# Kernel optimization log

Hardware: AMD Instinct MI355X
Metric: run time of the kernel (lower is better)

The kernel has to match this reference:

```python
import jax, jax.numpy as jnp
import numpy as np

N_NODES = 50000

def gcn_conv(x, src, dst, W, b):
    # x: [N, F_in], src/dst: [E], W: [F_in, F_out], b: [F_out]
    n = x.shape[0]
    xw = x @ W  # [N, F_out]
    # degree including self-loop (counted on destination nodes, PyG convention)
    deg = jax.ops.segment_sum(jnp.ones(src.shape[0], xw.dtype), dst, num_segments=n) + 1.0
    dinv = jax.lax.rsqrt(deg)  # deg >= 1 always
    norm = dinv[src] * dinv[dst]  # [E]
    msgs = xw[src] * norm[:, None]  # [E, F_out] gather + scale
    agg = jax.ops.segment_sum(msgs, dst, num_segments=n)  # scatter-add
    agg = agg + xw * (dinv * dinv)[:, None]  # self-loop contribution
    return agg + b


def setup_inputs() -> dict:
    key = jax.random.key(0)
    ks = jax.random.split(key, 8)
    n, e = N_NODES, 800000
    c_in, c_hid, c_out = 128, 128, 64
    x = jax.random.normal(ks[0], (n, c_in), dtype=jnp.float32)
    edge_index = jax.random.randint(ks[1], (2, e), 0, n, dtype=jnp.int64)
    s = 1.0 / np.sqrt(c_in)
    W1 = jax.random.uniform(ks[2], (c_in, c_hid), jnp.float32, -s, s)
    b1 = jnp.zeros((c_hid,), jnp.float32)
    sh = 1.0 / np.sqrt(c_hid)
    W2 = jax.random.uniform(ks[3], (c_hid, c_hid), jnp.float32, -sh, sh)
    b2 = jnp.zeros((c_hid,), jnp.float32)
    W3 = jax.random.uniform(ks[4], (c_hid, c_out), jnp.float32, -sh, sh)
    b3 = jnp.zeros((c_out,), jnp.float32)
    return {"x": x, "edge_index": edge_index, "W1": W1, "b1": b1,
            "W2": W2, "b2": b2, "W3": W3, "b3": b3}


def reference(x, edge_index, W1, b1, W2, b2, W3, b3):
    src, dst = edge_index[0], edge_index[1]
    h = gcn_conv(x, src, dst, W1, b1)
    h = gcn_conv(h, src, dst, W2, b2)
    h = gcn_conv(h, src, dst, W3, b3)
    return jax.nn.relu(h)  # activation applied after last layer only
```

## Files before the change

### kernel.cpp

```cpp
#include <hip/hip_runtime.h>
#include <hip/hip_fp16.h>


#define C_IN 128
#define C_HID 128
#define C_OUT 64
#define PART_BLOCKS 256
#define GEMM_BLOCKS 1024


__global__ __launch_bounds__(256) void buk_hist_kernel(const int* __restrict__ dst, int E,
                                                       int* __restrict__ bukCnt) {
    __shared__ int h[256];
    int tid = threadIdx.x;
    h[tid] = 0;
    __syncthreads();
    int chunk = (E + gridDim.x - 1) / gridDim.x;
    int lo = blockIdx.x * chunk;
    int hi = min(lo + chunk, E);
    for (int e = lo + tid; e < hi; e += 256)
        atomicAdd(&h[dst[e] >> 8], 1);
    __syncthreads();
    if (h[tid] > 0) atomicAdd(&bukCnt[tid], h[tid]);
}

__global__ __launch_bounds__(256) void buk_scan_kernel(const int* __restrict__ bukCnt,
                                                       int nbuk, int E,
                                                       int* __restrict__ bbase,
                                                       int* __restrict__ cursor) {
    __shared__ int lds[256];
    int tid = threadIdx.x;
    int v = (tid < nbuk) ? bukCnt[tid] : 0;
    lds[tid] = v;
    __syncthreads();
    for (int off = 1; off < 256; off <<= 1) {
        int u = (tid >= off) ? lds[tid - off] : 0;
        __syncthreads();
        lds[tid] += u;
        __syncthreads();
    }
    int ex = lds[tid] - v;
    if (tid < nbuk) { bbase[tid] = ex; cursor[tid] = ex; }
    if (tid == 0) bbase[nbuk] = E;
}

__global__ __launch_bounds__(256) void buk_place_kernel(const int* __restrict__ src,
                                                        const int* __restrict__ dst, int E,
                                                        int* __restrict__ cursor,
                                                        int2* __restrict__ ebuf) {
    __shared__ int h[256];
    __shared__ int base[256];
    __shared__ int c2[256];
    int tid = threadIdx.x;
    h[tid] = 0;
    c2[tid] = 0;
    __syncthreads();
    int chunk = (E + gridDim.x - 1) / gridDim.x;
    int lo = blockIdx.x * chunk;
    int hi = min(lo + chunk, E);
    for (int e = lo + tid; e < hi; e += 256)
        atomicAdd(&h[dst[e] >> 8], 1);
    __syncthreads();
    int cnt = h[tid];
    if (cnt > 0) base[tid] = atomicAdd(&cursor[tid], cnt);
    __syncthreads();
    for (int e = lo + tid; e < hi; e += 256) {
        int d = dst[e];
        int b = d >> 8;
        int slot = base[b] + atomicAdd(&c2[b], 1);
        ebuf[slot] = make_int2(src[e], d);
    }
}

__global__ __launch_bounds__(256) void buk_fill_kernel(const int2* __restrict__ ebuf,
                                                       const int* __restrict__ bbase,
                                                       int n, int E,
                                                       int* __restrict__ rowptr,
                                                       float* __restrict__ dinv,
                                                       int* __restrict__ csr) {
    __shared__ int deg[256];
    __shared__ int lds[256];
    int b = blockIdx.x;
    int tid = threadIdx.x;
    int lo = bbase[b];
    int hi = bbase[b + 1];
    int node0 = b << 8;
    deg[tid] = 0;
    __syncthreads();
    for (int e = lo + tid; e < hi; e += 256)
        atomicAdd(&deg[ebuf[e].y & 255], 1);
    __syncthreads();
    int d = deg[tid];
    lds[tid] = d;
    __syncthreads();
    for (int off = 1; off < 256; off <<= 1) {
        int u = (tid >= off) ? lds[tid - off] : 0;
        __syncthreads();
        lds[tid] += u;
        __syncthreads();
    }
    int ex = lds[tid] - d;
    int node = node0 + tid;
    if (node < n) {
        rowptr[node] = lo + ex;
        dinv[node] = rsqrtf((float)d + 1.0f);
    }
    if (tid == 0)
        rowptr[min(node0 + 256, n)] = hi;
    __syncthreads();
    deg[tid] = lo + ex;
    __syncthreads();
    for (int e = lo + tid; e < hi; e += 256) {
        int2 ed = ebuf[e];
        int slot = atomicAdd(&deg[ed.y & 255], 1);
        csr[slot] = ed.x;
    }
}

template <int FOUT>
__global__ __launch_bounds__(256, 4) void gemm_k128(const float* __restrict__ X,
                                                    const float* __restrict__ W,
                                                    const float* __restrict__ dinv,
                                                    float* __restrict__ Y,
                                                    __half* __restrict__ Yh, int n) {
    constexpr int K = 128;
    constexpr int CT = 64;
    constexpr int MT = 64;
    constexpr int NQ = CT / 4;
    constexpr int RPT = 4;
    constexpr int CTILES = FOUT / CT;
    __shared__ float Ws[K][CT];

    int tid = threadIdx.x;
    int ct = (CTILES == 1) ? 0 : (blockIdx.x & (CTILES - 1));
    int col0 = ct * CT;

#pragma unroll
    for (int i = 0; i < (K * CT / 4) / 256; ++i) {
        int idx = tid + i * 256;
        int k = idx / (CT / 4);
        int c = idx % (CT / 4);
        *(float4*)&Ws[k][c * 4] = *(const float4*)(W + (size_t)k * FOUT + col0 + c * 4);
    }
    __syncthreads();

    int cq = tid % NQ;
    int rg = tid / NQ;
    int nRowTiles = (n + MT - 1) / MT;
    int rtStride = gridDim.x / CTILES;

    for (int rt = blockIdx.x / CTILES; rt < nRowTiles; rt += rtStride) {
        int r0 = rt * MT + rg * RPT;

        const float* xb[RPT];
#pragma unroll
        for (int r = 0; r < RPT; ++r) {
            int gr = r0 + r;
            if (gr > n - 1) gr = n - 1;
            xb[r] = X + (size_t)gr * K;
        }

        float acc[RPT][4] = {};
        float4 xa[RPT];
#pragma unroll
        for (int r = 0; r < RPT; ++r) xa[r] = *(const float4*)(xb[r]);

#pragma unroll 2
        for (int k4 = 0; k4 < K / 4; ++k4) {
            float4 xn[RPT];
            if (k4 + 1 < K / 4) {
#pragma unroll
                for (int r = 0; r < RPT; ++r)
                    xn[r] = *(const float4*)(xb[r] + (k4 + 1) * 4);
            }
#pragma unroll
            for (int kk = 0; kk < 4; ++kk) {
                float4 w = *(float4*)&Ws[k4 * 4 + kk][cq * 4];
#pragma unroll
                for (int r = 0; r < RPT; ++r) {
                    float xarr[4] = {xa[r].x, xa[r].y, xa[r].z, xa[r].w};
                    float xv = xarr[kk];
                    acc[r][0] = fmaf(xv, w.x, acc[r][0]);
                    acc[r][1] = fmaf(xv, w.y, acc[r][1]);
                    acc[r][2] = fmaf(xv, w.z, acc[r][2]);
                    acc[r][3] = fmaf(xv, w.w, acc[r][3]);
                }
            }
#pragma unroll
            for (int r = 0; r < RPT; ++r) xa[r] = xn[r];
        }
#pragma unroll
        for (int r = 0; r < RPT; ++r) {
            int gr = r0 + r;
            if (gr < n) {
                size_t off = (size_t)gr * FOUT + col0 + cq * 4;
                *(float4*)(Y + off) =
                    make_float4(acc[r][0], acc[r][1], acc[r][2], acc[r][3]);
                float di = dinv[gr];
                __half2 h01 = __floats2half2_rn(acc[r][0] * di, acc[r][1] * di);
                __half2 h23 = __floats2half2_rn(acc[r][2] * di, acc[r][3] * di);
                uint2 pk = make_uint2(*(unsigned int*)&h01, *(unsigned int*)&h23);
                *(uint2*)(Yh + off) = pk;
            }
        }
    }
}

template <int NB, bool MASK>
__device__ __forceinline__ void batch_f128(const int* __restrict__ csr, int j, int rem,
                                           const __half* __restrict__ xwh, int lane,
                                           float2* acc) {
    int s[NB];
#pragma unroll
    for (int k = 0; k < NB; ++k) {
        int jj = MASK ? (j + ((k < rem) ? k : 0)) : (j + k);
        s[k] = csr[jj];
    }
    float2 v[NB];
#pragma unroll
    for (int k = 0; k < NB; ++k) {
        __half2 hv = ((const __half2*)(xwh + (size_t)s[k] * 128))[lane];
        v[k] = __half22float2(hv);
    }
#pragma unroll
    for (int k = 0; k < NB; ++k) {
        float m = (!MASK || (k < rem)) ? 1.0f : 0.0f;
        acc[k & 3].x = fmaf(v[k].x, m, acc[k & 3].x);
        acc[k & 3].y = fmaf(v[k].y, m, acc[k & 3].y);
    }
}

template <int NB, bool MASK>
__device__ __forceinline__ void batch_f64(const int* __restrict__ csr, int j, int rem,
                                          const __half* __restrict__ xwh, int lane,
                                          float* acc) {
    int s[NB];
#pragma unroll
    for (int k = 0; k < NB; ++k) {
        int jj = MASK ? (j + ((k < rem) ? k : 0)) : (j + k);
        s[k] = csr[jj];
    }
    float v[NB];
#pragma unroll
    for (int k = 0; k < NB; ++k)
        v[k] = __half2float(xwh[(size_t)s[k] * 64 + lane]);
#pragma unroll
    for (int k = 0; k < NB; ++k) {
        float m = (!MASK || (k < rem)) ? 1.0f : 0.0f;
        acc[k & 3] = fmaf(v[k], m, acc[k & 3]);
    }
}

template <int F, bool RELU>
__global__ __launch_bounds__(256) void agg_kernel(const int* __restrict__ rowptr,
                                                  const int* __restrict__ csr,
                                                  const float* __restrict__ xw,
                                                  const __half* __restrict__ xwh,
                                                  const float* __restrict__ dinv,
                                                  const float* __restrict__ bias,
                                                  float* __restrict__ out, int n) {
    int wave = threadIdx.x >> 6;
    int lane = threadIdx.x & 63;
    int i0 = blockIdx.x * 4 + wave;
    if (i0 >= n) return;
    int i = __builtin_amdgcn_readfirstlane(i0);
    float di = dinv[i];
    float d2 = di * di;
    int j = rowptr[i];
    int end = rowptr[i + 1];
    j = __builtin_amdgcn_readfirstlane(j);
    end = __builtin_amdgcn_readfirstlane(end);

    if constexpr (F == 128) {
        float2 x0 = ((const float2*)(xw + (size_t)i * F))[lane];
        float2 acc[4];
        acc[0] = acc[1] = acc[2] = acc[3] = make_float2(0.f, 0.f);

        for (; j + 16 <= end; j += 16) batch_f128<16, false>(csr, j, 0, xwh, lane, acc);
        if (j + 8 <= end) { batch_f128<8, false>(csr, j, 0, xwh, lane, acc); j += 8; }
        if (j + 4 <= end) { batch_f128<4, false>(csr, j, 0, xwh, lane, acc); j += 4; }
        int rem = end - j;
        if (rem > 0) batch_f128<4, true>(csr, j, rem, xwh, lane, acc);

        float2 bv = ((const float2*)bias)[lane];
        float2 o;
        o.x = fmaf(di, (acc[0].x + acc[1].x) + (acc[2].x + acc[3].x),
                   fmaf(x0.x, d2, bv.x));
        o.y = fmaf(di, (acc[0].y + acc[1].y) + (acc[2].y + acc[3].y),
                   fmaf(x0.y, d2, bv.y));
        if (RELU) { o.x = fmaxf(o.x, 0.f); o.y = fmaxf(o.y, 0.f); }
        ((float2*)(out + (size_t)i * F))[lane] = o;
    } else {
        float x0 = xw[(size_t)i * F + lane];
        float acc[4] = {0.f, 0.f, 0.f, 0.f};

        for (; j + 16 <= end; j += 16) batch_f64<16, false>(csr, j, 0, xwh, lane, acc);
        if (j + 8 <= end) { batch_f64<8, false>(csr, j, 0, xwh, lane, acc); j += 8; }
        if (j + 4 <= end) { batch_f64<4, false>(csr, j, 0, xwh, lane, acc); j += 4; }
        int rem = end - j;
        if (rem > 0) batch_f64<4, true>(csr, j, rem, xwh, lane, acc);

        float o = fmaf(di, (acc[0] + acc[1]) + (acc[2] + acc[3]),
                       fmaf(x0, d2, bias[lane]));
        if (RELU) o = fmaxf(o, 0.f);
        out[(size_t)i * F + lane] = o;
    }
}

extern "C" void kernel_launch(void* const* d_in, const int* in_sizes, int n_in,
                              void* d_out, int out_size, void* d_ws, size_t ws_size,
                              hipStream_t stream) {
    const float* x  = (const float*)d_in[0];
    const int*   ei = (const int*)d_in[1];
    const float* W1 = (const float*)d_in[2];
    const float* b1 = (const float*)d_in[3];
    const float* W2 = (const float*)d_in[4];
    const float* b2 = (const float*)d_in[5];
    const float* W3 = (const float*)d_in[6];
    const float* b3 = (const float*)d_in[7];
    float* out = (float*)d_out;

    int E = in_sizes[1] / 2;
    int n = in_sizes[0] / C_IN;
    const int* src = ei;
    const int* dst = ei + E;
    int nbuk = (n + 255) >> 8;

    float*  A        = (float*)d_ws;
    float*  B        = A + (size_t)n * C_HID;
    __half* Ah       = (__half*)(B + (size_t)n * C_HID);
    int2*   ebuf     = (int2*)(Ah + (size_t)n * C_HID);
    int*    csr      = (int*)(ebuf + E);
    float*  dinv     = (float*)(csr + E);
    int*    rowptr   = (int*)(dinv + n);
    int*    bukCnt   = rowptr + n + 1;
    int*    bbase    = bukCnt + 256;
    int*    cursor   = bbase + 256 + 1;

    hipMemsetAsync(bukCnt, 0, 256 * sizeof(int), stream);
    buk_hist_kernel<<<PART_BLOCKS, 256, 0, stream>>>(dst, E, bukCnt);
    buk_scan_kernel<<<1, 256, 0, stream>>>(bukCnt, nbuk, E, bbase, cursor);
    buk_place_kernel<<<PART_BLOCKS, 256, 0, stream>>>(src, dst, E, cursor, ebuf);
    buk_fill_kernel<<<nbuk, 256, 0, stream>>>(ebuf, bbase, n, E, rowptr, dinv, csr);

    int aggBlocks = (n + 3) / 4;

    gemm_k128<C_HID><<<GEMM_BLOCKS, 256, 0, stream>>>(x, W1, dinv, A, Ah, n);
    agg_kernel<C_HID, false><<<aggBlocks, 256, 0, stream>>>(rowptr, csr, A, Ah, dinv, b1, B, n);
    gemm_k128<C_HID><<<GEMM_BLOCKS, 256, 0, stream>>>(B, W2, dinv, A, Ah, n);
    agg_kernel<C_HID, false><<<aggBlocks, 256, 0, stream>>>(rowptr, csr, A, Ah, dinv, b2, B, n);
    gemm_k128<C_OUT><<<GEMM_BLOCKS, 256, 0, stream>>>(B, W3, dinv, A, Ah, n);
    agg_kernel<C_OUT, true><<<aggBlocks, 256, 0, stream>>>(rowptr, csr, A, Ah, dinv, b3, out, n);
}
```

Baseline: 305.8 us.

## Replace FP32 GEMMs with split-bf16 MFMA and emit hi/lo bf16 from aggregation

Replaces the scalar FP32 FMA GEMM with a bf16 MFMA kernel that uses a three-term hi/lo split (hi*hi + hi*lo + lo*hi) to approximate FP32 accuracy. The aggregation kernels now write their outputs directly as bf16 hi/lo pairs for the next GEMM, and a new split kernel converts the input features. The aim is to move the dense transforms onto matrix cores and shrink the bytes the GEMMs read. In exchange it adds an extra conversion pass, a per-block weight conversion into LDS, scalar (uncoalesced-width) output stores, and a small loss of precision versus FP32.

New measurement: 293.1 us. 1.04x faster.

```diff
diff --git a/kernel.cpp b/kernel.cpp
--- a/kernel.cpp
+++ b/kernel.cpp
@@ -6,7 +6,18 @@
 #define C_HID 128
 #define C_OUT 64
 #define PART_BLOCKS 256
-#define GEMM_BLOCKS 1024
+
+typedef __attribute__((ext_vector_type(8))) short bf16x8;
+typedef __attribute__((ext_vector_type(4))) float f32x4;
+
+__device__ __forceinline__ unsigned short bf16_rne(float f) {
+    unsigned u = __float_as_uint(f);
+    unsigned r = u + 0x7FFFu + ((u >> 16) & 1u);
+    return (unsigned short)(r >> 16);
+}
+__device__ __forceinline__ float bf16_f(unsigned short h) {
+    return __uint_as_float(((unsigned)h) << 16);
+}
 
 
 __global__ __launch_bounds__(256) void buk_hist_kernel(const int* __restrict__ dst, int E,
@@ -117,90 +128,111 @@
     }
 }
 
+__global__ __launch_bounds__(256) void split_kernel(const float* __restrict__ X,
+                                                    unsigned short* __restrict__ Hi,
+                                                    unsigned short* __restrict__ Lo,
+                                                    int total4) {
+    int g = blockIdx.x * blockDim.x + threadIdx.x;
+    if (g >= total4) return;
+    float4 v = ((const float4*)X)[g];
+    float vv[4] = {v.x, v.y, v.z, v.w};
+    unsigned short h[4], l[4];
+#pragma unroll
+    for (int i = 0; i < 4; ++i) {
+        h[i] = bf16_rne(vv[i]);
+        l[i] = bf16_rne(vv[i] - bf16_f(h[i]));
+    }
+    uint2 ph = make_uint2((unsigned)h[0] | ((unsigned)h[1] << 16),
+                          (unsigned)h[2] | ((unsigned)h[3] << 16));
+    uint2 pl = make_uint2((unsigned)l[0] | ((unsigned)l[1] << 16),
+                          (unsigned)l[2] | ((unsigned)l[3] << 16));
+    ((uint2*)Hi)[g] = ph;
+    ((uint2*)Lo)[g] = pl;
+}
+
 template <int FOUT>
-__global__ __launch_bounds__(256, 4) void gemm_k128(const float* __restrict__ X,
+__global__ __launch_bounds__(256, 2) void gemm_mfma(const unsigned short* __restrict__ Xhi,
+                                                    const unsigned short* __restrict__ Xlo,
                                                     const float* __restrict__ W,
                                                     const float* __restrict__ dinv,
                                                     float* __restrict__ Y,
                                                     __half* __restrict__ Yh, int n) {
-    constexpr int K = 128;
     constexpr int CT = 64;
-    constexpr int MT = 64;
-    constexpr int NQ = CT / 4;
-    constexpr int RPT = 4;
     constexpr int CTILES = FOUT / CT;
-    __shared__ float Ws[K][CT];
+    __shared__ unsigned short Bf[2][4][4][64][8];
 
     int tid = threadIdx.x;
-    int ct = (CTILES == 1) ? 0 : (blockIdx.x & (CTILES - 1));
+    int wv = tid >> 6, lane = tid & 63;
+    int ct = (CTILES == 1) ? 0 : (blockIdx.x % CTILES);
+    int rt = blockIdx.x / CTILES;
     int col0 = ct * CT;
-
-#pragma unroll
-    for (int i = 0; i < (K * CT / 4) / 256; ++i) {
-        int idx = tid + i * 256;
-        int k = idx / (CT / 4);
-        int c = idx % (CT / 4);
-        *(float4*)&Ws[k][c * 4] = *(const float4*)(W + (size_t)k * FOUT + col0 + c * 4);
-    }
-    __syncthreads();
-
-    int cq = tid % NQ;
-    int rg = tid / NQ;
-    int nRowTiles = (n + MT - 1) / MT;
-    int rtStride = gridDim.x / CTILES;
-
-    for (int rt = blockIdx.x / CTILES; rt < nRowTiles; rt += rtStride) {
-        int r0 = rt * MT + rg * RPT;
-
-        const float* xb[RPT];
-#pragma unroll
-        for (int r = 0; r < RPT; ++r) {
-            int gr = r0 + r;
-            if (gr > n - 1) gr = n - 1;
-            xb[r] = X + (size_t)gr * K;
+    int row0 = rt * 64 + wv * 16;
+
+    int rA = row0 + (lane & 15);
+    if (rA > n - 1) rA = n - 1;
+    const unsigned short* ph = Xhi + (size_t)rA * 128 + ((lane >> 4) * 8);
+    const unsigned short* pl = Xlo + (size_t)rA * 128 + ((lane >> 4) * 8);
+    bf16x8 ah[4], al[4];
+#pragma unroll
+    for (int kt = 0; kt < 4; ++kt) {
+        ah[kt] = *(const bf16x8*)(ph + kt * 32);
+        al[kt] = *(const bf16x8*)(pl + kt * 32);
+    }
+
+#pragma unroll
+    for (int i = 0; i < 8; ++i) {
+        int rid = tid + i * 256;
+        int set = rid >> 10;
+        int rem = rid & 1023;
+        int fr = rem >> 6;
+        int ln = rem & 63;
+        int kt = fr >> 2, nt = fr & 3;
+        int kbase = kt * 32 + (ln >> 4) * 8;
+        int cc = col0 + nt * 16 + (ln & 15);
+        unsigned short tmp[8];
+#pragma unroll
+        for (int j = 0; j < 8; ++j) {
+            float w = W[(size_t)(kbase + j) * FOUT + cc];
+            unsigned short hh = bf16_rne(w);
+            tmp[j] = (set == 0) ? hh : bf16_rne(w - bf16_f(hh));
         }
-
-        float acc[RPT][4] = {};
-        float4 xa[RPT];
-#pragma unroll
-        for (int r = 0; r < RPT; ++r) xa[r] = *(const float4*)(xb[r]);
-
-#pragma unroll 2
-        for (int k4 = 0; k4 < K / 4; ++k4) {
-            float4 xn[RPT];
-            if (k4 + 1 < K / 4) {
-#pragma unroll
-                for (int r = 0; r < RPT; ++r)
-                    xn[r] = *(const float4*)(xb[r] + (k4 + 1) * 4);
-            }
-#pragma unroll
-            for (int kk = 0; kk < 4; ++kk) {
-                float4 w = *(float4*)&Ws[k4 * 4 + kk][cq * 4];
-#pragma unroll
-                for (int r = 0; r < RPT; ++r) {
-                    float xarr[4] = {xa[r].x, xa[r].y, xa[r].z, xa[r].w};
-                    float xv = xarr[kk];
-                    acc[r][0] = fmaf(xv, w.x, acc[r][0]);
-                    acc[r][1] = fmaf(xv, w.y, acc[r][1]);
-                    acc[r][2] = fmaf(xv, w.z, acc[r][2]);
-                    acc[r][3] = fmaf(xv, w.w, acc[r][3]);
-                }
-            }
-#pragma unroll
-            for (int r = 0; r < RPT; ++r) xa[r] = xn[r];
+        *(bf16x8*)&Bf[set][kt][nt][ln][0] = *(bf16x8*)tmp;
+    }
+    __syncthreads();
+
+    bf16x8 bh[4][4], bl[4][4];
+#pragma unroll
+    for (int kt = 0; kt < 4; ++kt)
+#pragma unroll
+        for (int nt = 0; nt < 4; ++nt) {
+            bh[kt][nt] = *(const bf16x8*)&Bf[0][kt][nt][lane][0];
+            bl[kt][nt] = *(const bf16x8*)&Bf[1][kt][nt][lane][0];
         }
-#pragma unroll
-        for (int r = 0; r < RPT; ++r) {
-            int gr = r0 + r;
-            if (gr < n) {
-                size_t off = (size_t)gr * FOUT + col0 + cq * 4;
-                *(float4*)(Y + off) =
-                    make_float4(acc[r][0], acc[r][1], acc[r][2], acc[r][3]);
-                float di = dinv[gr];
-                __half2 h01 = __floats2half2_rn(acc[r][0] * di, acc[r][1] * di);
-                __half2 h23 = __floats2half2_rn(acc[r][2] * di, acc[r][3] * di);
-                uint2 pk = make_uint2(*(unsigned int*)&h01, *(unsigned int*)&h23);
-                *(uint2*)(Yh + off) = pk;
+
+    f32x4 acc[4];
+#pragma unroll
+    for (int nt = 0; nt < 4; ++nt) acc[nt] = (f32x4){0.f, 0.f, 0.f, 0.f};
+
+#pragma unroll
+    for (int kt = 0; kt < 4; ++kt)
+#pragma unroll
+        for (int nt = 0; nt < 4; ++nt) {
+            acc[nt] = __builtin_amdgcn_mfma_f32_16x16x32_bf16(ah[kt], bh[kt][nt], acc[nt], 0, 0, 0);
+            acc[nt] = __builtin_amdgcn_mfma_f32_16x16x32_bf16(ah[kt], bl[kt][nt], acc[nt], 0, 0, 0);
+            acc[nt] = __builtin_amdgcn_mfma_f32_16x16x32_bf16(al[kt], bh[kt][nt], acc[nt], 0, 0, 0);
+        }
+
+#pragma unroll
+    for (int r = 0; r < 4; ++r) {
+        int grow = row0 + (lane >> 4) * 4 + r;
+        if (grow < n) {
+            float di = dinv[grow];
+#pragma unroll
+            for (int nt = 0; nt < 4; ++nt) {
+                float v = acc[nt][r];
+                size_t off = (size_t)grow * FOUT + col0 + nt * 16 + (lane & 15);
+                Y[off] = v;
+                Yh[off] = __float2half(v * di);
             }
         }
     }
@@ -251,14 +283,17 @@
     }
 }
 
-template <int F, bool RELU>
+template <int F, int MODE>
 __global__ __launch_bounds__(256) void agg_kernel(const int* __restrict__ rowptr,
                                                   const int* __restrict__ csr,
                                                   const float* __restrict__ xw,
                                                   const __half* __restrict__ xwh,
                                                   const float* __restrict__ dinv,
                                                   const float* __restrict__ bias,
-                                                  float* __restrict__ out, int n) {
+                                                  float* __restrict__ out,
+                                                  unsigned short* __restrict__ outHi,
+                                                  unsigned short* __restrict__ outLo,
+                                                  int n) {
     int wave = threadIdx.x >> 6;
     int lane = threadIdx.x & 63;
     int i0 = blockIdx.x * 4 + wave;
@@ -283,13 +318,16 @@
         if (rem > 0) batch_f128<4, true>(csr, j, rem, xwh, lane, acc);
 
         float2 bv = ((const float2*)bias)[lane];
-        float2 o;
-        o.x = fmaf(di, (acc[0].x + acc[1].x) + (acc[2].x + acc[3].x),
-                   fmaf(x0.x, d2, bv.x));
-        o.y = fmaf(di, (acc[0].y + acc[1].y) + (acc[2].y + acc[3].y),
-                   fmaf(x0.y, d2, bv.y));
-        if (RELU) { o.x = fmaxf(o.x, 0.f); o.y = fmaxf(o.y, 0.f); }
-        ((float2*)(out + (size_t)i * F))[lane] = o;
+        float ox = fmaf(di, (acc[0].x + acc[1].x) + (acc[2].x + acc[3].x),
+                        fmaf(x0.x, d2, bv.x));
+        float oy = fmaf(di, (acc[0].y + acc[1].y) + (acc[2].y + acc[3].y),
+                        fmaf(x0.y, d2, bv.y));
+        unsigned short h0 = bf16_rne(ox);
+        unsigned short l0 = bf16_rne(ox - bf16_f(h0));
+        unsigned short h1 = bf16_rne(oy);
+        unsigned short l1 = bf16_rne(oy - bf16_f(h1));
+        ((unsigned*)(outHi + (size_t)i * F))[lane] = (unsigned)h0 | ((unsigned)h1 << 16);
+        ((unsigned*)(outLo + (size_t)i * F))[lane] = (unsigned)l0 | ((unsigned)l1 << 16);
     } else {
         float x0 = xw[(size_t)i * F + lane];
         float acc[4] = {0.f, 0.f, 0.f, 0.f};
@@ -302,7 +340,7 @@
 
         float o = fmaf(di, (acc[0] + acc[1]) + (acc[2] + acc[3]),
                        fmaf(x0, d2, bias[lane]));
-        if (RELU) o = fmaxf(o, 0.f);
+        o = fmaxf(o, 0.f);
         out[(size_t)i * F + lane] = o;
     }
 }
@@ -326,16 +364,17 @@
     const int* dst = ei + E;
     int nbuk = (n + 255) >> 8;
 
-    float*  A        = (float*)d_ws;
-    float*  B        = A + (size_t)n * C_HID;
-    __half* Ah       = (__half*)(B + (size_t)n * C_HID);
-    int2*   ebuf     = (int2*)(Ah + (size_t)n * C_HID);
-    int*    csr      = (int*)(ebuf + E);
-    float*  dinv     = (float*)(csr + E);
-    int*    rowptr   = (int*)(dinv + n);
-    int*    bukCnt   = rowptr + n + 1;
-    int*    bbase    = bukCnt + 256;
-    int*    cursor   = bbase + 256 + 1;
+    float*          A    = (float*)d_ws;
+    __half*         Ah   = (__half*)(A + (size_t)n * C_HID);
+    unsigned short* Bhi  = (unsigned short*)(Ah + (size_t)n * C_HID);
+    unsigned short* Blo  = Bhi + (size_t)n * C_HID;
+    int2*           ebuf = (int2*)(Blo + (size_t)n * C_HID);
+    int*            csr  = (int*)(ebuf + E);
+    float*          dinv = (float*)(csr + E);
+    int*            rowptr = (int*)(dinv + n);
+    int*            bukCnt = rowptr + n + 1;
+    int*            bbase  = bukCnt + 256;
+    int*            cursor = bbase + 256 + 1;
 
     hipMemsetAsync(bukCnt, 0, 256 * sizeof(int), stream);
     buk_hist_kernel<<<PART_BLOCKS, 256, 0, stream>>>(dst, E, bukCnt);
@@ -343,12 +382,19 @@
     buk_place_kernel<<<PART_BLOCKS, 256, 0, stream>>>(src, dst, E, cursor, ebuf);
     buk_fill_kernel<<<nbuk, 256, 0, stream>>>(ebuf, bbase, n, E, rowptr, dinv, csr);
 
+    int total4 = n * C_IN / 4;
+    split_kernel<<<(total4 + 255) / 256, 256, 0, stream>>>(x, Bhi, Blo, total4);
+
     int aggBlocks = (n + 3) / 4;
-
-    gemm_k128<C_HID><<<GEMM_BLOCKS, 256, 0, stream>>>(x, W1, dinv, A, Ah, n);
-    agg_kernel<C_HID, false><<<aggBlocks, 256, 0, stream>>>(rowptr, csr, A, Ah, dinv, b1, B, n);
-    gemm_k128<C_HID><<<GEMM_BLOCKS, 256, 0, stream>>>(B, W2, dinv, A, Ah, n);
-    agg_kernel<C_HID, false><<<aggBlocks, 256, 0, stream>>>(rowptr, csr, A, Ah, dinv, b2, B, n);
-    gemm_k128<C_OUT><<<GEMM_BLOCKS, 256, 0, stream>>>(B, W3, dinv, A, Ah, n);
-    agg_kernel<C_OUT, true><<<aggBlocks, 256, 0, stream>>>(rowptr, csr, A, Ah, dinv, b3, out, n);
-}
+    int rowTiles = (n + 63) / 64;
+
+    gemm_mfma<C_HID><<<rowTiles * 2, 256, 0, stream>>>(Bhi, Blo, W1, dinv, A, Ah, n);
+    agg_kernel<C_HID, 0><<<aggBlocks, 256, 0, stream>>>(rowptr, csr, A, Ah, dinv, b1,
+                                                        nullptr, Bhi, Blo, n);
+    gemm_mfma<C_HID><<<rowTiles * 2, 256, 0, stream>>>(Bhi, Blo, W2, dinv, A, Ah, n);
+    agg_kernel<C_HID, 0><<<aggBlocks, 256, 0, stream>>>(rowptr, csr, A, Ah, dinv, b2,
+                                                        nullptr, Bhi, Blo, n);
+    gemm_mfma<C_OUT><<<rowTiles, 256, 0, stream>>>(Bhi, Blo, W3, dinv, A, Ah, n);
+    agg_kernel<C_OUT, 1><<<aggBlocks, 256, 0, stream>>>(rowptr, csr, A, Ah, dinv, b3,
+                                                        out, nullptr, nullptr, n);
+}
```
